# Kernel tuning notes

Hardware: AMD Instinct MI355X
Metric: run time of the kernel (lower is better)

The kernel has to match this reference:

```python
import jax, jax.numpy as jnp
import numpy as np

N_NODES = 20000
N_EDGES = 160000
IN_DIM = 512
HID = 256
N_CLASSES = 2
NUM_GRAPHS = 16


def setup_inputs() -> dict:
    key = jax.random.key(0)
    ks = jax.random.split(key, 12)
    x = jax.random.normal(ks[0], (N_NODES, IN_DIM), dtype=jnp.float32)
    edge_index = jax.random.randint(ks[1], (2, N_EDGES), 0, N_NODES, dtype=jnp.int64)
    batch = jnp.sort(jax.random.randint(ks[2], (N_NODES,), 0, NUM_GRAPHS, dtype=jnp.int64))
    def glorot(k, shape):
        lim = float(np.sqrt(6.0 / (shape[0] + shape[1])))
        return jax.random.uniform(k, shape, jnp.float32, -lim, lim)
    return {
        "x": x,
        "edge_index": edge_index,
        "batch": batch,
        "W1n": glorot(ks[3], (IN_DIM, HID)),
        "W1s": glorot(ks[4], (IN_DIM, HID)),
        "b1": jnp.zeros((HID,), jnp.float32),
        "W2n": glorot(ks[5], (HID, HID)),
        "W2s": glorot(ks[6], (HID, HID)),
        "b2": jnp.zeros((HID,), jnp.float32),
        "fc1w": glorot(ks[7], (HID, HID // 2)),
        "fc1b": jnp.zeros((HID // 2,), jnp.float32),
        "fc2w": glorot(ks[8], (HID // 2, N_CLASSES)),
        "fc2b": jnp.zeros((N_CLASSES,), jnp.float32),
    }


def _sage_conv(x, W_nbr, W_self, b, src, dst, n_nodes):
    # mean-aggregate neighbor features (messages flow src -> dst, PyG convention)
    deg = jax.ops.segment_sum(jnp.ones(src.shape, x.dtype), dst, num_segments=n_nodes)
    deg = jnp.maximum(deg, 1.0)
    aggr = jax.ops.segment_sum(x[src], dst, num_segments=n_nodes) / deg[:, None]
    # SAGEConv: lin_l(aggr) + lin_r(x) + bias (equivalent to concat-linear)
    return aggr @ W_nbr + x @ W_self + b


def reference(x, edge_index, batch, W1n, W1s, b1, W2n, W2s, b2, fc1w, fc1b, fc2w, fc2b):
    src, dst = edge_index[0], edge_index[1]
    n = x.shape[0]
    h = jax.nn.relu(_sage_conv(x, W1n, W1s, b1, src, dst, n))
    h = jax.nn.relu(_sage_conv(h, W2n, W2s, b2, src, dst, n))
    # global_mean_pool over graph ids
    cnt = jax.ops.segment_sum(jnp.ones((n,), h.dtype), batch, num_segments=NUM_GRAPHS)
    pooled = jax.ops.segment_sum(h, batch, num_segments=NUM_GRAPHS) / jnp.maximum(cnt, 1.0)[:, None]
    out = jax.nn.relu(pooled @ fc1w + fc1b) @ fc2w + fc2b
    return out
```

## Files before the change

kernel.cpp:

```cpp
#include <hip/hip_runtime.h>
#include <hip/hip_bf16.h>


#define HID 256
#define NCOL 512

typedef __bf16 bf16x8 __attribute__((ext_vector_type(8)));
typedef float floatx4 __attribute__((ext_vector_type(4)));
typedef unsigned int u32;
typedef const u32 __attribute__((address_space(1)))* gp_t;
typedef u32 __attribute__((address_space(3)))* lp_t;

__device__ __forceinline__ ushort f2bf(float f) {
    unsigned u = __float_as_uint(f);
    u += 0x7fffu + ((u >> 16) & 1u);
    return (ushort)(u >> 16);
}
__device__ __forceinline__ float bf2f(ushort b) {
    return __uint_as_float(((unsigned)b) << 16);
}

__global__ void cvt_kernel(const float* __restrict__ in, ushort* __restrict__ out, int n4) {
    int i = blockIdx.x * 256 + threadIdx.x;
    if (i >= n4) return;
    float4 v = ((const float4*)in)[i];
    ushort4 o;
    o.x = f2bf(v.x); o.y = f2bf(v.y); o.z = f2bf(v.z); o.w = f2bf(v.w);
    ((ushort4*)out)[i] = o;
}

__global__ void packT_kernel(const float* __restrict__ Wn, const float* __restrict__ Ws,
                             ushort* __restrict__ WT, int K) {
    int gid = blockIdx.x * 256 + threadIdx.x;
    if (gid >= NCOL * K) return;
    int n = gid / K, k = gid - n * K;
    float v = (n < HID) ? Wn[k * HID + n] : Ws[k * HID + (n - HID)];
    WT[gid] = f2bf(v);
}

__global__ void degi_kernel(const int* __restrict__ dst, int* __restrict__ degi, int n_edges) {
    int e = blockIdx.x * 256 + threadIdx.x;
    if (e < n_edges) atomicAdd(&degi[dst[e]], 1);
}

__global__ __launch_bounds__(256) void psum_kernel(const int* __restrict__ degi,
                                                   int* __restrict__ partials, int n) {
    int t = threadIdx.x;
    int i = blockIdx.x * 256 + t;
    int v = (i < n) ? degi[i] : 0;
#pragma unroll
    for (int d = 1; d < 64; d <<= 1) v += __shfl_xor(v, d, 64);
    __shared__ int wsum[4];
    if ((t & 63) == 0) wsum[t >> 6] = v;
    __syncthreads();
    if (t == 0) partials[blockIdx.x] = wsum[0] + wsum[1] + wsum[2] + wsum[3];
}

__global__ __launch_bounds__(64) void pscan_kernel(int* __restrict__ partials,
                                                   int* __restrict__ off, int nb, int n) {
    int lane = threadIdx.x;
    int carry = 0;
    for (int base = 0; base < nb; base += 256) {
        int i0 = base + lane * 4;
        int v0 = (i0 + 0 < nb) ? partials[i0 + 0] : 0;
        int v1 = (i0 + 1 < nb) ? partials[i0 + 1] : 0;
        int v2 = (i0 + 2 < nb) ? partials[i0 + 2] : 0;
        int v3 = (i0 + 3 < nb) ? partials[i0 + 3] : 0;
        int local = v0 + v1 + v2 + v3;
        int s = local;
#pragma unroll
        for (int d = 1; d < 64; d <<= 1) {
            int t = __shfl_up(s, d, 64);
            if (lane >= d) s += t;
        }
        int excl = carry + s - local;
        if (i0 + 0 < nb) partials[i0 + 0] = excl;
        excl += v0;
        if (i0 + 1 < nb) partials[i0 + 1] = excl;
        excl += v1;
        if (i0 + 2 < nb) partials[i0 + 2] = excl;
        excl += v2;
        if (i0 + 3 < nb) partials[i0 + 3] = excl;
        carry += __shfl(s, 63, 64);
    }
    if (lane == 0) off[n] = carry;
}

__global__ __launch_bounds__(256) void scan2_kernel(const int* __restrict__ degi,
                                                    const int* __restrict__ partials,
                                                    int* __restrict__ off,
                                                    int* __restrict__ cursor, int n) {
    int t = threadIdx.x, lane = t & 63, w = t >> 6;
    int i = blockIdx.x * 256 + t;
    int v = (i < n) ? degi[i] : 0;
    int s = v;
#pragma unroll
    for (int d = 1; d < 64; d <<= 1) {
        int u = __shfl_up(s, d, 64);
        if (lane >= d) s += u;
    }
    __shared__ int wsum[4];
    if (lane == 63) wsum[w] = s;
    __syncthreads();
    int woff = 0;
    for (int k = 0; k < w; ++k) woff += wsum[k];
    int excl = partials[blockIdx.x] + woff + s - v;
    if (i < n) { off[i] = excl; cursor[i] = excl; }
}

__global__ void fill_kernel(const int* __restrict__ src, const int* __restrict__ dst,
                            int* __restrict__ cursor, int* __restrict__ eidx, int n_edges) {
    int e = blockIdx.x * 256 + threadIdx.x;
    if (e < n_edges) {
        int p = atomicAdd(&cursor[dst[e]], 1);
        eidx[p] = src[e];
    }
}

__global__ __launch_bounds__(256) void gemm_mfma(const ushort* __restrict__ A,
                                                 const ushort* __restrict__ BT,
                                                 ushort* __restrict__ Ynb,
                                                 float* __restrict__ Ys, int K) {
    __shared__ ushort As[2][128 * 64];
    __shared__ ushort Bs[2][128 * 64];
    int tid = threadIdx.x;
    int w = tid >> 6, lane = tid & 63;
    int quad = lane >> 4, r16 = lane & 15;
    int m0 = blockIdx.y * 128, n0 = blockIdx.x * 128;
    int wm = (w >> 1) * 64, wn = (w & 1) * 64;

    int srow[4], sgu[4];
#pragma unroll
    for (int rr = 0; rr < 4; ++rr) {
        int idx = rr * 256 + tid;
        srow[rr] = idx >> 3;
        sgu[rr] = (idx & 7) ^ (srow[rr] & 7);
    }

    auto stage = [&](int buf, int k0) {
#pragma unroll
        for (int rr = 0; rr < 4; ++rr) {
            const ushort* ga = A + (size_t)(m0 + srow[rr]) * K + k0 + sgu[rr] * 8;
            const ushort* gb = BT + (size_t)(n0 + srow[rr]) * K + k0 + sgu[rr] * 8;
            ushort* la = As[buf] + (size_t)(rr * 256 + w * 64) * 8;
            ushort* lb = Bs[buf] + (size_t)(rr * 256 + w * 64) * 8;
            __builtin_amdgcn_global_load_lds((gp_t)(const void*)ga, (lp_t)(void*)la, 16, 0, 0);
            __builtin_amdgcn_global_load_lds((gp_t)(const void*)gb, (lp_t)(void*)lb, 16, 0, 0);
        }
    };

    floatx4 acc[4][4];
#pragma unroll
    for (int i = 0; i < 4; ++i)
#pragma unroll
        for (int j = 0; j < 4; ++j) acc[i][j] = (floatx4){0.f, 0.f, 0.f, 0.f};

    const int nk = K >> 6;
    stage(0, 0);
    for (int t = 0; t < nk; ++t) {
        int cb = t & 1;
        __syncthreads();
        if (t + 1 < nk) stage(cb ^ 1, (t + 1) << 6);
        const ushort* Ab = As[cb];
        const ushort* Bb = Bs[cb];
#pragma unroll
        for (int s = 0; s < 2; ++s) {
            bf16x8 a[4], b[4];
#pragma unroll
            for (int i = 0; i < 4; ++i) {
                int row = wm + i * 16 + r16;
                int au = (s * 4 + quad) ^ (row & 7);
                a[i] = *(const bf16x8*)(Ab + row * 64 + au * 8);
            }
#pragma unroll
            for (int j = 0; j < 4; ++j) {
                int row = wn + j * 16 + r16;
                int bu = (s * 4 + quad) ^ (row & 7);
                b[j] = *(const bf16x8*)(Bb + row * 64 + bu * 8);
            }
#pragma unroll
            for (int i = 0; i < 4; ++i)
#pragma unroll
                for (int j = 0; j < 4; ++j)
                    acc[i][j] = __builtin_amdgcn_mfma_f32_16x16x32_bf16(a[i], b[j], acc[i][j], 0, 0, 0);
        }
    }
    bool isYn = (n0 + wn) < HID;
#pragma unroll
    for (int i = 0; i < 4; ++i)
#pragma unroll
        for (int j = 0; j < 4; ++j) {
            int col16 = n0 + wn + j * 16 + r16;
#pragma unroll
            for (int rg = 0; rg < 4; ++rg) {
                int row = m0 + wm + i * 16 + quad * 4 + rg;
                if (isYn) Ynb[(size_t)row * HID + col16] = f2bf(acc[i][j][rg]);
                else      Ys[(size_t)row * HID + (col16 - HID)] = acc[i][j][rg];
            }
        }
}

__global__ __launch_bounds__(256) void gather_kernel(const ushort* __restrict__ Ynb,
                                                     const float* __restrict__ Ys,
                                                     const int* __restrict__ off,
                                                     const int* __restrict__ eidx,
                                                     const float* __restrict__ bias,
                                                     ushort* __restrict__ h, int n_nodes) {
    int tid = threadIdx.x;
    int v = blockIdx.x * 4 + (tid >> 6);
    if (v >= n_nodes) return;
    int q4 = (tid & 63) << 2;
    int e0 = off[v], e1 = off[v + 1];
    float4 acc0 = make_float4(0.f, 0.f, 0.f, 0.f);
    float4 acc1 = make_float4(0.f, 0.f, 0.f, 0.f);
    int e = e0;
    for (; e + 1 < e1; e += 2) {
        int s0 = eidx[e], s1 = eidx[e + 1];
        ushort4 y0 = *(const ushort4*)(Ynb + (size_t)s0 * HID + q4);
        ushort4 y1 = *(const ushort4*)(Ynb + (size_t)s1 * HID + q4);
        acc0.x += bf2f(y0.x); acc0.y += bf2f(y0.y);
        acc0.z += bf2f(y0.z); acc0.w += bf2f(y0.w);
        acc1.x += bf2f(y1.x); acc1.y += bf2f(y1.y);
        acc1.z += bf2f(y1.z); acc1.w += bf2f(y1.w);
    }
    if (e < e1) {
        ushort4 y = *(const ushort4*)(Ynb + (size_t)eidx[e] * HID + q4);
        acc0.x += bf2f(y.x); acc0.y += bf2f(y.y);
        acc0.z += bf2f(y.z); acc0.w += bf2f(y.w);
    }
    float invd = 1.0f / fmaxf((float)(e1 - e0), 1.0f);
    float4 s = *(const float4*)(Ys + (size_t)v * HID + q4);
    float4 b = *(const float4*)(bias + q4);
    ushort4 r;
    r.x = f2bf(fmaxf((acc0.x + acc1.x) * invd + s.x + b.x, 0.f));
    r.y = f2bf(fmaxf((acc0.y + acc1.y) * invd + s.y + b.y, 0.f));
    r.z = f2bf(fmaxf((acc0.z + acc1.z) * invd + s.z + b.z, 0.f));
    r.w = f2bf(fmaxf((acc0.w + acc1.w) * invd + s.w + b.w, 0.f));
    *(ushort4*)(h + (size_t)v * HID + q4) = r;
}

__global__ void pool_kernel(const ushort* __restrict__ h, const int* __restrict__ batch,
                            float* __restrict__ pooled, float* __restrict__ cnt, int n_nodes) {
    int f = threadIdx.x;
    int v0 = blockIdx.x * 64;
    int vend = min(v0 + 64, n_nodes);
    if (v0 >= n_nodes) return;
    int cur = batch[v0];
    float acc = 0.f, ac = 0.f;
    for (int v = v0; v < vend; ++v) {
        int g = batch[v];
        if (g != cur) {
            atomicAdd(&pooled[cur * HID + f], acc);
            if (f == 0) atomicAdd(&cnt[cur], ac);
            acc = 0.f; ac = 0.f; cur = g;
        }
        acc += bf2f(h[(size_t)v * HID + f]);
        ac += 1.0f;
    }
    atomicAdd(&pooled[cur * HID + f], acc);
    if (f == 0) atomicAdd(&cnt[cur], ac);
}

__global__ void head_kernel(const float* __restrict__ pooled, const float* __restrict__ cnt,
                            const float* __restrict__ fc1w, const float* __restrict__ fc1b,
                            const float* __restrict__ fc2w, const float* __restrict__ fc2b,
                            float* __restrict__ out) {
    int g = blockIdx.x, j = threadIdx.x;
    __shared__ float p[256];
    __shared__ float hid[128];
    float inv = 1.0f / fmaxf(cnt[g], 1.0f);
    p[j] = pooled[g * HID + j] * inv;
    p[j + 128] = pooled[g * HID + 128 + j] * inv;
    __syncthreads();
    float a = fc1b[j];
    for (int f = 0; f < 256; ++f) a += p[f] * fc1w[f * 128 + j];
    hid[j] = fmaxf(a, 0.f);
    __syncthreads();
    if (j < 2) {
        float o = fc2b[j];
        for (int t = 0; t < 128; ++t) o += hid[t] * fc2w[t * 2 + j];
        out[g * 2 + j] = o;
    }
}

extern "C" void kernel_launch(void* const* d_in, const int* in_sizes, int n_in,
                              void* d_out, int out_size, void* d_ws, size_t ws_size,
                              hipStream_t stream) {
    const float* x    = (const float*)d_in[0];
    const int*   ei   = (const int*)d_in[1];
    const int*   batch= (const int*)d_in[2];
    const float* W1n  = (const float*)d_in[3];
    const float* W1s  = (const float*)d_in[4];
    const float* b1   = (const float*)d_in[5];
    const float* W2n  = (const float*)d_in[6];
    const float* W2s  = (const float*)d_in[7];
    const float* b2   = (const float*)d_in[8];
    const float* fc1w = (const float*)d_in[9];
    const float* fc1b = (const float*)d_in[10];
    const float* fc2w = (const float*)d_in[11];
    const float* fc2b = (const float*)d_in[12];
    float* out = (float*)d_out;

    const int n_nodes = in_sizes[2];
    const int n_edges = in_sizes[1] / 2;
    const int in_dim  = in_sizes[0] / n_nodes;
    const int Mpad    = (n_nodes + 127) & ~127;
    const int nb      = (n_nodes + 255) / 256;
    const int* src = ei;
    const int* dst = ei + n_edges;

    char* wsb = (char*)d_ws;
    size_t cur = 0;
    auto alloc = [&](size_t nbytes) { size_t o = cur; cur = (cur + nbytes + 255) & ~(size_t)255; return o; };
    size_t o_degi = alloc((size_t)n_nodes * 4);
    size_t o_off  = alloc((size_t)(n_nodes + 1) * 4);
    size_t o_cur  = alloc((size_t)n_nodes * 4);
    size_t o_part = alloc((size_t)nb * 4);
    size_t o_eidx = alloc((size_t)n_edges * 4);
    size_t o_w1   = alloc((size_t)NCOL * in_dim * 2);
    size_t o_w2   = alloc((size_t)NCOL * HID * 2);
    size_t o_xb   = alloc((size_t)Mpad * in_dim * 2);
    size_t o_hb   = alloc((size_t)Mpad * HID * 2);
    size_t o_ynb  = alloc((size_t)Mpad * HID * 2);
    size_t o_ys   = alloc((size_t)Mpad * HID * 4);
    size_t o_pool = alloc((size_t)16 * HID * 4 + 16 * 4);
    (void)ws_size;

    int*    degi    = (int*)(wsb + o_degi);
    int*    off     = (int*)(wsb + o_off);
    int*    cursor  = (int*)(wsb + o_cur);
    int*    partials= (int*)(wsb + o_part);
    int*    eidx    = (int*)(wsb + o_eidx);
    ushort* w1t     = (ushort*)(wsb + o_w1);
    ushort* w2t     = (ushort*)(wsb + o_w2);
    ushort* xb      = (ushort*)(wsb + o_xb);
    ushort* hb      = (ushort*)(wsb + o_hb);
    ushort* Ynb     = (ushort*)(wsb + o_ynb);
    float*  Ys      = (float*)(wsb + o_ys);
    float*  pooled  = (float*)(wsb + o_pool);
    float*  cnt     = pooled + 16 * HID;

    hipMemsetAsync(degi, 0, (size_t)n_nodes * 4, stream);
    hipMemsetAsync(pooled, 0, (size_t)(16 * HID + 16) * 4, stream);

    degi_kernel<<<(n_edges + 255) / 256, 256, 0, stream>>>(dst, degi, n_edges);
    psum_kernel<<<nb, 256, 0, stream>>>(degi, partials, n_nodes);
    pscan_kernel<<<1, 64, 0, stream>>>(partials, off, nb, n_nodes);
    scan2_kernel<<<nb, 256, 0, stream>>>(degi, partials, off, cursor, n_nodes);
    fill_kernel<<<(n_edges + 255) / 256, 256, 0, stream>>>(src, dst, cursor, eidx, n_edges);

    int n4 = n_nodes * in_dim / 4;
    cvt_kernel<<<(n4 + 255) / 256, 256, 0, stream>>>(x, xb, n4);
    packT_kernel<<<(NCOL * in_dim + 255) / 256, 256, 0, stream>>>(W1n, W1s, w1t, in_dim);
    packT_kernel<<<(NCOL * HID + 255) / 256, 256, 0, stream>>>(W2n, W2s, w2t, HID);

    dim3 gemm_grid(NCOL / 128, Mpad / 128);
    int gather_blocks = (n_nodes + 3) / 4;

    gemm_mfma<<<gemm_grid, 256, 0, stream>>>(xb, w1t, Ynb, Ys, in_dim);
    gather_kernel<<<gather_blocks, 256, 0, stream>>>(Ynb, Ys, off, eidx, b1, hb, n_nodes);

    gemm_mfma<<<gemm_grid, 256, 0, stream>>>(hb, w2t, Ynb, Ys, HID);
    gather_kernel<<<gather_blocks, 256, 0, stream>>>(Ynb, Ys, off, eidx, b2, hb, n_nodes);

    pool_kernel<<<(n_nodes + 63) / 64, 256, 0, stream>>>(hb, batch, pooled, cnt, n_nodes);
    head_kernel<<<16, 128, 0, stream>>>(pooled, cnt, fc1w, fc1b, fc2w, fc2b, out);
}
```

Measured before the change: 251.9 us.

## Fuse prep kernels, shrink GEMM M-tile, store bf16 interleaved Y, unroll gather

Merges the x conversion, the two weight pack/transposes and the degree count into one prep launch, which saves launch overhead. The GEMM M-tile shrinks from 128 to 64 rows, doubling the block count for better CU occupancy on a small M. The neighbor and self projections now go to one bf16 buffer with row stride 512, so the self term is no longer stored in fp32. The gather loop is unrolled by 4 for more memory-level parallelism. The self term is now rounded to bf16, which slightly reduces precision.

```diff
diff --git a/kernel.cpp b/kernel.cpp
--- a/kernel.cpp
+++ b/kernel.cpp
@@ -20,27 +20,39 @@
     return __uint_as_float(((unsigned)b) << 16);
 }
 
-__global__ void cvt_kernel(const float* __restrict__ in, ushort* __restrict__ out, int n4) {
-    int i = blockIdx.x * 256 + threadIdx.x;
-    if (i >= n4) return;
-    float4 v = ((const float4*)in)[i];
-    ushort4 o;
-    o.x = f2bf(v.x); o.y = f2bf(v.y); o.z = f2bf(v.z); o.w = f2bf(v.w);
-    ((ushort4*)out)[i] = o;
-}
-
-__global__ void packT_kernel(const float* __restrict__ Wn, const float* __restrict__ Ws,
-                             ushort* __restrict__ WT, int K) {
-    int gid = blockIdx.x * 256 + threadIdx.x;
+__device__ __forceinline__ void packT_work(const float* __restrict__ Wn,
+                                           const float* __restrict__ Ws,
+                                           ushort* __restrict__ WT, int K, int gid) {
     if (gid >= NCOL * K) return;
     int n = gid / K, k = gid - n * K;
     float v = (n < HID) ? Wn[k * HID + n] : Ws[k * HID + (n - HID)];
     WT[gid] = f2bf(v);
 }
 
-__global__ void degi_kernel(const int* __restrict__ dst, int* __restrict__ degi, int n_edges) {
-    int e = blockIdx.x * 256 + threadIdx.x;
-    if (e < n_edges) atomicAdd(&degi[dst[e]], 1);
+__global__ void prep_kernel(const float* __restrict__ x, ushort* __restrict__ xb, int n4,
+                            const float* __restrict__ W1n, const float* __restrict__ W1s,
+                            ushort* __restrict__ w1t, int K1,
+                            const float* __restrict__ W2n, const float* __restrict__ W2s,
+                            ushort* __restrict__ w2t, int K2,
+                            const int* __restrict__ dst, int* __restrict__ degi, int n_edges,
+                            int nb_cvt, int nb_w1, int nb_w2) {
+    int bx = blockIdx.x, t = threadIdx.x;
+    if (bx < nb_cvt) {
+        int i = bx * 256 + t;
+        if (i < n4) {
+            float4 v = ((const float4*)x)[i];
+            ushort4 o;
+            o.x = f2bf(v.x); o.y = f2bf(v.y); o.z = f2bf(v.z); o.w = f2bf(v.w);
+            ((ushort4*)xb)[i] = o;
+        }
+    } else if (bx < nb_cvt + nb_w1) {
+        packT_work(W1n, W1s, w1t, K1, (bx - nb_cvt) * 256 + t);
+    } else if (bx < nb_cvt + nb_w1 + nb_w2) {
+        packT_work(W2n, W2s, w2t, K2, (bx - nb_cvt - nb_w1) * 256 + t);
+    } else {
+        int e = (bx - nb_cvt - nb_w1 - nb_w2) * 256 + t;
+        if (e < n_edges) atomicAdd(&degi[dst[e]], 1);
+    }
 }
 
 __global__ __launch_bounds__(256) void psum_kernel(const int* __restrict__ degi,
@@ -119,39 +131,47 @@
 
 __global__ __launch_bounds__(256) void gemm_mfma(const ushort* __restrict__ A,
                                                  const ushort* __restrict__ BT,
-                                                 ushort* __restrict__ Ynb,
-                                                 float* __restrict__ Ys, int K) {
-    __shared__ ushort As[2][128 * 64];
+                                                 ushort* __restrict__ Y, int K) {
+    __shared__ ushort As[2][64 * 64];
     __shared__ ushort Bs[2][128 * 64];
     int tid = threadIdx.x;
     int w = tid >> 6, lane = tid & 63;
     int quad = lane >> 4, r16 = lane & 15;
-    int m0 = blockIdx.y * 128, n0 = blockIdx.x * 128;
-    int wm = (w >> 1) * 64, wn = (w & 1) * 64;
-
-    int srow[4], sgu[4];
+    int m0 = blockIdx.y * 64, n0 = blockIdx.x * 128;
+    int wm = (w >> 1) * 32, wn = (w & 1) * 64;
+
+    int arow[2], agu[2], brow[4], bgu[4];
+#pragma unroll
+    for (int rr = 0; rr < 2; ++rr) {
+        int idx = rr * 256 + tid;
+        arow[rr] = idx >> 3;
+        agu[rr] = (idx & 7) ^ (arow[rr] & 7);
+    }
 #pragma unroll
     for (int rr = 0; rr < 4; ++rr) {
         int idx = rr * 256 + tid;
-        srow[rr] = idx >> 3;
-        sgu[rr] = (idx & 7) ^ (srow[rr] & 7);
+        brow[rr] = idx >> 3;
+        bgu[rr] = (idx & 7) ^ (brow[rr] & 7);
     }
 
     auto stage = [&](int buf, int k0) {
 #pragma unroll
+        for (int rr = 0; rr < 2; ++rr) {
+            const ushort* ga = A + (size_t)(m0 + arow[rr]) * K + k0 + agu[rr] * 8;
+            ushort* la = As[buf] + (size_t)(rr * 256 + w * 64) * 8;
+            __builtin_amdgcn_global_load_lds((gp_t)(const void*)ga, (lp_t)(void*)la, 16, 0, 0);
+        }
+#pragma unroll
         for (int rr = 0; rr < 4; ++rr) {
-            const ushort* ga = A + (size_t)(m0 + srow[rr]) * K + k0 + sgu[rr] * 8;
-            const ushort* gb = BT + (size_t)(n0 + srow[rr]) * K + k0 + sgu[rr] * 8;
-            ushort* la = As[buf] + (size_t)(rr * 256 + w * 64) * 8;
+            const ushort* gb = BT + (size_t)(n0 + brow[rr]) * K + k0 + bgu[rr] * 8;
             ushort* lb = Bs[buf] + (size_t)(rr * 256 + w * 64) * 8;
-            __builtin_amdgcn_global_load_lds((gp_t)(const void*)ga, (lp_t)(void*)la, 16, 0, 0);
             __builtin_amdgcn_global_load_lds((gp_t)(const void*)gb, (lp_t)(void*)lb, 16, 0, 0);
         }
     };
 
-    floatx4 acc[4][4];
-#pragma unroll
-    for (int i = 0; i < 4; ++i)
+    floatx4 acc[2][4];
+#pragma unroll
+    for (int i = 0; i < 2; ++i)
 #pragma unroll
         for (int j = 0; j < 4; ++j) acc[i][j] = (floatx4){0.f, 0.f, 0.f, 0.f};
 
@@ -165,9 +185,9 @@
         const ushort* Bb = Bs[cb];
 #pragma unroll
         for (int s = 0; s < 2; ++s) {
-            bf16x8 a[4], b[4];
-#pragma unroll
-            for (int i = 0; i < 4; ++i) {
+            bf16x8 a[2], b[4];
+#pragma unroll
+            for (int i = 0; i < 2; ++i) {
                 int row = wm + i * 16 + r16;
                 int au = (s * 4 + quad) ^ (row & 7);
                 a[i] = *(const bf16x8*)(Ab + row * 64 + au * 8);
@@ -179,29 +199,26 @@
                 b[j] = *(const bf16x8*)(Bb + row * 64 + bu * 8);
             }
 #pragma unroll
-            for (int i = 0; i < 4; ++i)
+            for (int i = 0; i < 2; ++i)
 #pragma unroll
                 for (int j = 0; j < 4; ++j)
                     acc[i][j] = __builtin_amdgcn_mfma_f32_16x16x32_bf16(a[i], b[j], acc[i][j], 0, 0, 0);
         }
     }
-    bool isYn = (n0 + wn) < HID;
-#pragma unroll
-    for (int i = 0; i < 4; ++i)
+#pragma unroll
+    for (int i = 0; i < 2; ++i)
 #pragma unroll
         for (int j = 0; j < 4; ++j) {
-            int col16 = n0 + wn + j * 16 + r16;
+            int col = n0 + wn + j * 16 + r16;
 #pragma unroll
             for (int rg = 0; rg < 4; ++rg) {
                 int row = m0 + wm + i * 16 + quad * 4 + rg;
-                if (isYn) Ynb[(size_t)row * HID + col16] = f2bf(acc[i][j][rg]);
-                else      Ys[(size_t)row * HID + (col16 - HID)] = acc[i][j][rg];
+                Y[(size_t)row * NCOL + col] = f2bf(acc[i][j][rg]);
             }
         }
 }
 
-__global__ __launch_bounds__(256) void gather_kernel(const ushort* __restrict__ Ynb,
-                                                     const float* __restrict__ Ys,
+__global__ __launch_bounds__(256) void gather_kernel(const ushort* __restrict__ Y,
                                                      const int* __restrict__ off,
                                                      const int* __restrict__ eidx,
                                                      const float* __restrict__ bias,
@@ -211,31 +228,31 @@
     if (v >= n_nodes) return;
     int q4 = (tid & 63) << 2;
     int e0 = off[v], e1 = off[v + 1];
-    float4 acc0 = make_float4(0.f, 0.f, 0.f, 0.f);
-    float4 acc1 = make_float4(0.f, 0.f, 0.f, 0.f);
+    ushort4 sv = *(const ushort4*)(Y + (size_t)v * NCOL + HID + q4);
+    float4 b = *(const float4*)(bias + q4);
+    float4 a0 = make_float4(0.f, 0.f, 0.f, 0.f), a1 = a0, a2 = a0, a3 = a0;
     int e = e0;
-    for (; e + 1 < e1; e += 2) {
-        int s0 = eidx[e], s1 = eidx[e + 1];
-        ushort4 y0 = *(const ushort4*)(Ynb + (size_t)s0 * HID + q4);
-        ushort4 y1 = *(const ushort4*)(Ynb + (size_t)s1 * HID + q4);
-        acc0.x += bf2f(y0.x); acc0.y += bf2f(y0.y);
-        acc0.z += bf2f(y0.z); acc0.w += bf2f(y0.w);
-        acc1.x += bf2f(y1.x); acc1.y += bf2f(y1.y);
-        acc1.z += bf2f(y1.z); acc1.w += bf2f(y1.w);
-    }
-    if (e < e1) {
-        ushort4 y = *(const ushort4*)(Ynb + (size_t)eidx[e] * HID + q4);
-        acc0.x += bf2f(y.x); acc0.y += bf2f(y.y);
-        acc0.z += bf2f(y.z); acc0.w += bf2f(y.w);
+    for (; e + 3 < e1; e += 4) {
+        int s0 = eidx[e], s1 = eidx[e + 1], s2 = eidx[e + 2], s3 = eidx[e + 3];
+        ushort4 y0 = *(const ushort4*)(Y + (size_t)s0 * NCOL + q4);
+        ushort4 y1 = *(const ushort4*)(Y + (size_t)s1 * NCOL + q4);
+        ushort4 y2 = *(const ushort4*)(Y + (size_t)s2 * NCOL + q4);
+        ushort4 y3 = *(const ushort4*)(Y + (size_t)s3 * NCOL + q4);
+        a0.x += bf2f(y0.x); a0.y += bf2f(y0.y); a0.z += bf2f(y0.z); a0.w += bf2f(y0.w);
+        a1.x += bf2f(y1.x); a1.y += bf2f(y1.y); a1.z += bf2f(y1.z); a1.w += bf2f(y1.w);
+        a2.x += bf2f(y2.x); a2.y += bf2f(y2.y); a2.z += bf2f(y2.z); a2.w += bf2f(y2.w);
+        a3.x += bf2f(y3.x); a3.y += bf2f(y3.y); a3.z += bf2f(y3.z); a3.w += bf2f(y3.w);
+    }
+    for (; e < e1; ++e) {
+        ushort4 y = *(const ushort4*)(Y + (size_t)eidx[e] * NCOL + q4);
+        a0.x += bf2f(y.x); a0.y += bf2f(y.y); a0.z += bf2f(y.z); a0.w += bf2f(y.w);
     }
     float invd = 1.0f / fmaxf((float)(e1 - e0), 1.0f);
-    float4 s = *(const float4*)(Ys + (size_t)v * HID + q4);
-    float4 b = *(const float4*)(bias + q4);
     ushort4 r;
-    r.x = f2bf(fmaxf((acc0.x + acc1.x) * invd + s.x + b.x, 0.f));
-    r.y = f2bf(fmaxf((acc0.y + acc1.y) * invd + s.y + b.y, 0.f));
-    r.z = f2bf(fmaxf((acc0.z + acc1.z) * invd + s.z + b.z, 0.f));
-    r.w = f2bf(fmaxf((acc0.w + acc1.w) * invd + s.w + b.w, 0.f));
+    r.x = f2bf(fmaxf((a0.x + a1.x + a2.x + a3.x) * invd + bf2f(sv.x) + b.x, 0.f));
+    r.y = f2bf(fmaxf((a0.y + a1.y + a2.y + a3.y) * invd + bf2f(sv.y) + b.y, 0.f));
+    r.z = f2bf(fmaxf((a0.z + a1.z + a2.z + a3.z) * invd + bf2f(sv.z) + b.z, 0.f));
+    r.w = f2bf(fmaxf((a0.w + a1.w + a2.w + a3.w) * invd + bf2f(sv.w) + b.w, 0.f));
     *(ushort4*)(h + (size_t)v * HID + q4) = r;
 }
 
@@ -304,7 +321,7 @@
     const int n_nodes = in_sizes[2];
     const int n_edges = in_sizes[1] / 2;
     const int in_dim  = in_sizes[0] / n_nodes;
-    const int Mpad    = (n_nodes + 127) & ~127;
+    const int Mpad    = (n_nodes + 63) & ~63;
     const int nb      = (n_nodes + 255) / 256;
     const int* src = ei;
     const int* dst = ei + n_edges;
@@ -321,8 +338,7 @@
     size_t o_w2   = alloc((size_t)NCOL * HID * 2);
     size_t o_xb   = alloc((size_t)Mpad * in_dim * 2);
     size_t o_hb   = alloc((size_t)Mpad * HID * 2);
-    size_t o_ynb  = alloc((size_t)Mpad * HID * 2);
-    size_t o_ys   = alloc((size_t)Mpad * HID * 4);
+    size_t o_y    = alloc((size_t)Mpad * NCOL * 2);
     size_t o_pool = alloc((size_t)16 * HID * 4 + 16 * 4);
     (void)ws_size;
 
@@ -335,33 +351,35 @@
     ushort* w2t     = (ushort*)(wsb + o_w2);
     ushort* xb      = (ushort*)(wsb + o_xb);
     ushort* hb      = (ushort*)(wsb + o_hb);
-    ushort* Ynb     = (ushort*)(wsb + o_ynb);
-    float*  Ys      = (float*)(wsb + o_ys);
+    ushort* Y       = (ushort*)(wsb + o_y);
     float*  pooled  = (float*)(wsb + o_pool);
     float*  cnt     = pooled + 16 * HID;
 
     hipMemsetAsync(degi, 0, (size_t)n_nodes * 4, stream);
     hipMemsetAsync(pooled, 0, (size_t)(16 * HID + 16) * 4, stream);
 
-    degi_kernel<<<(n_edges + 255) / 256, 256, 0, stream>>>(dst, degi, n_edges);
+    int n4 = n_nodes * in_dim / 4;
+    int nb_cvt = (n4 + 255) / 256;
+    int nb_w1  = (NCOL * in_dim + 255) / 256;
+    int nb_w2  = (NCOL * HID + 255) / 256;
+    int nb_deg = (n_edges + 255) / 256;
+    prep_kernel<<<nb_cvt + nb_w1 + nb_w2 + nb_deg, 256, 0, stream>>>(
+        x, xb, n4, W1n, W1s, w1t, in_dim, W2n, W2s, w2t, HID,
+        dst, degi, n_edges, nb_cvt, nb_w1, nb_w2);
+
     psum_kernel<<<nb, 256, 0, stream>>>(degi, partials, n_nodes);
     pscan_kernel<<<1, 64, 0, stream>>>(partials, off, nb, n_nodes);
     scan2_kernel<<<nb, 256, 0, stream>>>(degi, partials, off, cursor, n_nodes);
     fill_kernel<<<(n_edges + 255) / 256, 256, 0, stream>>>(src, dst, cursor, eidx, n_edges);
 
-    int n4 = n_nodes * in_dim / 4;
-    cvt_kernel<<<(n4 + 255) / 256, 256, 0, stream>>>(x, xb, n4);
-    packT_kernel<<<(NCOL * in_dim + 255) / 256, 256, 0, stream>>>(W1n, W1s, w1t, in_dim);
-    packT_kernel<<<(NCOL * HID + 255) / 256, 256, 0, stream>>>(W2n, W2s, w2t, HID);
-
-    dim3 gemm_grid(NCOL / 128, Mpad / 128);
+    dim3 gemm_grid(NCOL / 128, Mpad / 64);
     int gather_blocks = (n_nodes + 3) / 4;
 
-    gemm_mfma<<<gemm_grid, 256, 0, stream>>>(xb, w1t, Ynb, Ys, in_dim);
-    gather_kernel<<<gather_blocks, 256, 0, stream>>>(Ynb, Ys, off, eidx, b1, hb, n_nodes);
-
-    gemm_mfma<<<gemm_grid, 256, 0, stream>>>(hb, w2t, Ynb, Ys, HID);
-    gather_kernel<<<gather_blocks, 256, 0, stream>>>(Ynb, Ys, off, eidx, b2, hb, n_nodes);
+    gemm_mfma<<<gemm_grid, 256, 0, stream>>>(xb, w1t, Y, in_dim);
+    gather_kernel<<<gather_blocks, 256, 0, stream>>>(Y, off, eidx, b1, hb, n_nodes);
+
+    gemm_mfma<<<gemm_grid, 256, 0, stream>>>(hb, w2t, Y, HID);
+    gather_kernel<<<gather_blocks, 256, 0, stream>>>(Y, off, eidx, b2, hb, n_nodes);
 
     pool_kernel<<<(n_nodes + 63) / 64, 256, 0, stream>>>(hb, batch, pooled, cnt, n_nodes);
     head_kernel<<<16, 128, 0, stream>>>(pooled, cnt, fc1w, fc1b, fc2w, fc2b, out);
```

New measurement: 231.6 us. 1.09x faster.
